# Kernel optimization log

Hardware: AMD Instinct MI355X
Metric: run time of the kernel (lower is better)

Reference implementation:

```python
import jax, jax.numpy as jnp
import numpy as np

N = 50000      # nodes
E = 500000     # edges (includes N self-loops)
DIN = 512
DOUT = 256
NEG_SLOPE = 0.01  # torch nn.LeakyReLU default


def setup_inputs() -> dict:
    key = jax.random.key(0)
    k1, k2, k3, k4, k5 = jax.random.split(key, 5)
    x = jax.random.normal(k1, (N, DIN), dtype=jnp.float32)
    # xavier_normal_ with gain=1.414
    std_W = 1.414 * np.sqrt(2.0 / (DIN + DOUT))
    W = jax.random.normal(k2, (DIN, DOUT), dtype=jnp.float32) * std_W
    std_a = 1.414 * np.sqrt(2.0 / (1 + 2 * DOUT))
    a = jax.random.normal(k3, (2 * DOUT,), dtype=jnp.float32) * std_a
    # first N edges are self-loops so every row-sum is nonzero
    loops = jnp.arange(N, dtype=jnp.int32)
    edge_src = jnp.concatenate([loops, jax.random.randint(k4, (E - N,), 0, N, dtype=jnp.int32)])
    edge_dst = jnp.concatenate([loops, jax.random.randint(k5, (E - N,), 0, N, dtype=jnp.int32)])
    return {"x": x, "W": W, "a": a, "edge_src": edge_src, "edge_dst": edge_dst}


def reference(x, W, a, edge_src, edge_dst):
    n = x.shape[0]
    d = W.shape[1]
    h = x @ W  # [N, DOUT]
    # a . [h_src ; h_dst] decomposed per-node, then gathered per-edge
    s_src = h @ a[:d]   # [N]
    s_dst = h @ a[d:]   # [N]
    score = s_src[edge_src] + s_dst[edge_dst]          # [E]
    e = jnp.exp(-jax.nn.leaky_relu(score, NEG_SLOPE))  # [E]
    # sparse softmax denominator: spmm(edge, e, ones) == segment sum over src
    e_rowsum = jax.ops.segment_sum(e, edge_src, num_segments=n)            # [N]
    # numerator: spmm(edge, e, h) == sum_j e_ij * h_j per row i
    h_prime = jax.ops.segment_sum(e[:, None] * h[edge_dst], edge_src, num_segments=n)  # [N, DOUT]
    h_prime = h_prime / e_rowsum[:, None]
    return jax.nn.elu(h_prime)  # concat=True branch
```

## Files before the change

kernel.cpp:

```cpp
#include <hip/hip_runtime.h>
#include <math.h>

#define DIN 512
#define DOUT 256
#define NEG_SLOPE 0.01f

typedef __attribute__((ext_vector_type(8))) short bf16x8;
typedef __attribute__((ext_vector_type(4))) float f32x4;
typedef __attribute__((ext_vector_type(4))) unsigned int u32x4;

__device__ __forceinline__ unsigned short f2bf(float f) {
    unsigned int u = __float_as_uint(f);
    unsigned int r = (u + 0x7FFFu + ((u >> 16) & 1u)) >> 16;
    return (unsigned short)r;
}
__device__ __forceinline__ float bf2f(unsigned short u) {
    return __uint_as_float(((unsigned int)u) << 16);
}
__device__ __forceinline__ unsigned int cvtpk(float lo, float hi) {
    unsigned int r;
    asm("v_cvt_pk_bf16_f32 %0, %1, %2" : "=v"(r) : "v"(lo), "v"(hi));
    return r;
}

__global__ void prep(const float* __restrict__ W, unsigned short* __restrict__ Bp,
                     int* __restrict__ deg, float* __restrict__ s_src,
                     float* __restrict__ s_dst, int N) {
    int t = blockIdx.x * blockDim.x + threadIdx.x;
    if (t < (DIN / 32) * (DOUT / 16) * 64) {
        int lane = t & 63;
        int cg = (t >> 6) & 15;
        int ks = t >> 10;
        int l15 = lane & 15, g = lane >> 4;
        int col = cg * 16 + l15;
        int k0 = ks * 32 + g * 8;
        ushort4 lo, hi;
        lo.x = f2bf(W[(size_t)(k0 + 0) * DOUT + col]);
        lo.y = f2bf(W[(size_t)(k0 + 1) * DOUT + col]);
        lo.z = f2bf(W[(size_t)(k0 + 2) * DOUT + col]);
        lo.w = f2bf(W[(size_t)(k0 + 3) * DOUT + col]);
        hi.x = f2bf(W[(size_t)(k0 + 4) * DOUT + col]);
        hi.y = f2bf(W[(size_t)(k0 + 5) * DOUT + col]);
        hi.z = f2bf(W[(size_t)(k0 + 6) * DOUT + col]);
        hi.w = f2bf(W[(size_t)(k0 + 7) * DOUT + col]);
        *(ushort4*)(Bp + (size_t)t * 8) = lo;
        *(ushort4*)(Bp + (size_t)t * 8 + 4) = hi;
    }
    if (t < N) { deg[t] = 0; s_src[t] = 0.f; s_dst[t] = 0.f; }
}

__global__ __launch_bounds__(64, 2) void gemm_k(const float* __restrict__ x,
                                                const unsigned short* __restrict__ Bp,
                                                unsigned short* __restrict__ hb,
                                                const float* __restrict__ av,
                                                float* __restrict__ s_src,
                                                float* __restrict__ s_dst, int M) {
    const int lane = threadIdx.x;
    const int l15 = lane & 15;
    const int g = lane >> 4;
    const int m0 = blockIdx.x * 32;

    int r0 = min(m0 + l15, M - 1);
    int r1 = min(m0 + 16 + l15, M - 1);
    const float* pA0 = x + (size_t)r0 * DIN + g * 8;
    const float* pA1 = x + (size_t)r1 * DIN + g * 8;
    const unsigned short* pB = Bp + (size_t)lane * 8;

    f32x4 acc[2][16] = {};

#pragma unroll
    for (int ks = 0; ks < DIN / 32; ++ks) {
        f32x4 a00 = *(const f32x4*)(pA0 + ks * 32);
        f32x4 a01 = *(const f32x4*)(pA0 + ks * 32 + 4);
        f32x4 a10 = *(const f32x4*)(pA1 + ks * 32);
        f32x4 a11 = *(const f32x4*)(pA1 + ks * 32 + 4);
        u32x4 p;
        p.x = cvtpk(a00.x, a00.y); p.y = cvtpk(a00.z, a00.w);
        p.z = cvtpk(a01.x, a01.y); p.w = cvtpk(a01.z, a01.w);
        bf16x8 af0 = *(bf16x8*)&p;
        u32x4 q;
        q.x = cvtpk(a10.x, a10.y); q.y = cvtpk(a10.z, a10.w);
        q.z = cvtpk(a11.x, a11.y); q.w = cvtpk(a11.z, a11.w);
        bf16x8 af1 = *(bf16x8*)&q;
        const unsigned short* pBks = pB + (size_t)ks * 16 * 512;
#pragma unroll
        for (int cg = 0; cg < 16; ++cg) {
            bf16x8 bfr = *(const bf16x8*)(pBks + (size_t)cg * 512);
            acc[0][cg] = __builtin_amdgcn_mfma_f32_16x16x32_bf16(af0, bfr, acc[0][cg], 0, 0, 0);
            acc[1][cg] = __builtin_amdgcn_mfma_f32_16x16x32_bf16(af1, bfr, acc[1][cg], 0, 0, 0);
        }
    }

    float as_[16], ad_[16];
#pragma unroll
    for (int cg = 0; cg < 16; ++cg) {
        int col = cg * 16 + l15;
        as_[cg] = av[col];
        ad_[cg] = av[DOUT + col];
    }
#pragma unroll
    for (int rf = 0; rf < 2; ++rf) {
#pragma unroll
        for (int j = 0; j < 4; ++j) {
            int row = m0 + rf * 16 + g * 4 + j;
            float ps = 0.f, pd = 0.f;
#pragma unroll
            for (int cg = 0; cg < 16; ++cg) {
                float v = acc[rf][cg][j];
                ps += v * as_[cg];
                pd += v * ad_[cg];
            }
#pragma unroll
            for (int off = 1; off < 16; off <<= 1) {
                ps += __shfl_xor(ps, off);
                pd += __shfl_xor(pd, off);
            }
            if (row < M) {
#pragma unroll
                for (int cg = 0; cg < 16; ++cg)
                    hb[(size_t)row * DOUT + cg * 16 + l15] = f2bf(acc[rf][cg][j]);
                if (l15 == 0) {
                    atomicAdd(&s_src[row], ps);
                    atomicAdd(&s_dst[row], pd);
                }
            }
        }
    }
}

__global__ void hist_k(const int* __restrict__ src, int* __restrict__ deg, int E) {
    int i = blockIdx.x * blockDim.x + threadIdx.x;
    if (i < E) atomicAdd(&deg[src[i]], 1);
}

__global__ __launch_bounds__(256) void block_sum(const int* __restrict__ deg, int* __restrict__ bsum, int N) {
    __shared__ int wsum[4];
    int b = blockIdx.x, t = threadIdx.x;
    int idx = b * 1024 + t * 4;
    int s = 0;
    if (idx + 3 < N) {
        int4 v = *(const int4*)(deg + idx);
        s = v.x + v.y + v.z + v.w;
    } else {
        for (int i = 0; i < 4; i++) if (idx + i < N) s += deg[idx + i];
    }
#pragma unroll
    for (int off = 32; off > 0; off >>= 1) s += __shfl_xor(s, off);
    if ((t & 63) == 0) wsum[t >> 6] = s;
    __syncthreads();
    if (t == 0) bsum[b] = wsum[0] + wsum[1] + wsum[2] + wsum[3];
}

__global__ void scan_tops(const int* __restrict__ bsum, int* __restrict__ boff,
                          int* __restrict__ rowptr, int nb, int N, int E) {
    int t = threadIdx.x;
    int v = (t < nb) ? bsum[t] : 0;
    int x = v;
#pragma unroll
    for (int off = 1; off < 64; off <<= 1) {
        int y = __shfl_up(x, off);
        if (t >= off) x += y;
    }
    if (t < nb) boff[t] = x - v;
    if (t == 0) rowptr[N] = E;
}

__global__ __launch_bounds__(256) void scan_blk(const int* __restrict__ deg, const int* __restrict__ boff,
                                                int* __restrict__ rowptr, int* __restrict__ cursor, int N) {
    __shared__ int wsum[4];
    int b = blockIdx.x, t = threadIdx.x;
    int idx = b * 1024 + t * 4;
    int v0 = 0, v1 = 0, v2 = 0, v3 = 0;
    if (idx + 3 < N) {
        int4 v = *(const int4*)(deg + idx);
        v0 = v.x; v1 = v.y; v2 = v.z; v3 = v.w;
    } else if (idx < N) {
        v0 = deg[idx];
        if (idx + 1 < N) v1 = deg[idx + 1];
        if (idx + 2 < N) v2 = deg[idx + 2];
    }
    int s = v0 + v1 + v2 + v3;
    int lane = t & 63, wid = t >> 6;
    int x = s;
#pragma unroll
    for (int off = 1; off < 64; off <<= 1) {
        int y = __shfl_up(x, off);
        if (lane >= off) x += y;
    }
    if (lane == 63) wsum[wid] = x;
    __syncthreads();
    int add = boff[b];
    for (int ww = 0; ww < wid; ++ww) add += wsum[ww];
    int e0 = add + x - s;
    int e1 = e0 + v0, e2 = e1 + v1, e3 = e2 + v2;
    if (idx < N)     { rowptr[idx] = e0;     cursor[idx] = e0; }
    if (idx + 1 < N) { rowptr[idx + 1] = e1; cursor[idx + 1] = e1; }
    if (idx + 2 < N) { rowptr[idx + 2] = e2; cursor[idx + 2] = e2; }
    if (idx + 3 < N) { rowptr[idx + 3] = e3; cursor[idx + 3] = e3; }
}

__global__ void edge_k(const int* __restrict__ src, const int* __restrict__ dst,
                       const float* __restrict__ s_src, const float* __restrict__ s_dst,
                       int* __restrict__ cursor, int2* __restrict__ csr, int E) {
    int i = blockIdx.x * blockDim.x + threadIdx.x;
    if (i >= E) return;
    int s = src[i], d = dst[i];
    float sc = s_src[s] + s_dst[d];
    float lrv = sc > 0.f ? sc : NEG_SLOPE * sc;
    float ev = __expf(-lrv);
    int pos = atomicAdd(&cursor[s], 1);
    csr[pos] = make_int2(d, __float_as_int(ev));
}

__global__ __launch_bounds__(256) void gather_k(const unsigned short* __restrict__ hb,
                                                const int* __restrict__ rowptr,
                                                const int2* __restrict__ csr,
                                                float* __restrict__ out, int N) {
    int gt = blockIdx.x * blockDim.x + threadIdx.x;
    int w = gt >> 6;
    int lane = threadIdx.x & 63;
    if (w >= N) return;
    int s0 = rowptr[w], s1 = rowptr[w + 1];
    float a0 = 0.f, a1 = 0.f, a2 = 0.f, a3 = 0.f, rs = 0.f;
    for (int base = s0; base < s1; base += 64) {
        int cnt = min(64, s1 - base);
        int dv = 0; float ev = 0.f;
        if (lane < cnt) {
            int2 p = csr[base + lane];
            dv = p.x; ev = __int_as_float(p.y);
        }
        int jj = 0;
        for (; jj + 4 <= cnt; jj += 4) {
            int d0 = __shfl(dv, jj), d1 = __shfl(dv, jj + 1), d2 = __shfl(dv, jj + 2), d3 = __shfl(dv, jj + 3);
            float e0 = __shfl(ev, jj), e1 = __shfl(ev, jj + 1), e2 = __shfl(ev, jj + 2), e3 = __shfl(ev, jj + 3);
            ushort4 h0 = *(const ushort4*)(hb + (size_t)d0 * DOUT + lane * 4);
            ushort4 h1 = *(const ushort4*)(hb + (size_t)d1 * DOUT + lane * 4);
            ushort4 h2 = *(const ushort4*)(hb + (size_t)d2 * DOUT + lane * 4);
            ushort4 h3 = *(const ushort4*)(hb + (size_t)d3 * DOUT + lane * 4);
            a0 += e0 * bf2f(h0.x) + e1 * bf2f(h1.x) + e2 * bf2f(h2.x) + e3 * bf2f(h3.x);
            a1 += e0 * bf2f(h0.y) + e1 * bf2f(h1.y) + e2 * bf2f(h2.y) + e3 * bf2f(h3.y);
            a2 += e0 * bf2f(h0.z) + e1 * bf2f(h1.z) + e2 * bf2f(h2.z) + e3 * bf2f(h3.z);
            a3 += e0 * bf2f(h0.w) + e1 * bf2f(h1.w) + e2 * bf2f(h2.w) + e3 * bf2f(h3.w);
            rs += e0 + e1 + e2 + e3;
        }
        for (; jj < cnt; ++jj) {
            int d0 = __shfl(dv, jj);
            float e0 = __shfl(ev, jj);
            ushort4 h0 = *(const ushort4*)(hb + (size_t)d0 * DOUT + lane * 4);
            a0 += e0 * bf2f(h0.x);
            a1 += e0 * bf2f(h0.y);
            a2 += e0 * bf2f(h0.z);
            a3 += e0 * bf2f(h0.w);
            rs += e0;
        }
    }
    float inv = 1.f / rs;
    float4 v;
    v.x = a0 * inv; v.y = a1 * inv; v.z = a2 * inv; v.w = a3 * inv;
    v.x = v.x > 0.f ? v.x : __expf(v.x) - 1.f;
    v.y = v.y > 0.f ? v.y : __expf(v.y) - 1.f;
    v.z = v.z > 0.f ? v.z : __expf(v.z) - 1.f;
    v.w = v.w > 0.f ? v.w : __expf(v.w) - 1.f;
    *(float4*)(out + (size_t)w * DOUT + lane * 4) = v;
}

extern "C" void kernel_launch(void* const* d_in, const int* in_sizes, int n_in,
                              void* d_out, int out_size, void* d_ws, size_t ws_size,
                              hipStream_t stream) {
    const float* x = (const float*)d_in[0];
    const float* W = (const float*)d_in[1];
    const float* a = (const float*)d_in[2];
    const int* edge_src = (const int*)d_in[3];
    const int* edge_dst = (const int*)d_in[4];

    const int N = in_sizes[0] / DIN;
    const int E = in_sizes[3];
    const int nb = (N + 1023) / 1024;

    char* ws = (char*)d_ws;
    size_t off = 0;
    auto alloc = [&](size_t bytes) {
        void* p = ws + off;
        off += (bytes + 15) & ~(size_t)15;
        return p;
    };
    unsigned short* hb = (unsigned short*)alloc((size_t)N * DOUT * 2);
    unsigned short* Bp = (unsigned short*)alloc((size_t)DIN * DOUT * 2);
    int* rowptr = (int*)alloc((size_t)(N + 1) * 4);
    int* deg = (int*)alloc((size_t)N * 4);
    int* cursor = (int*)alloc((size_t)N * 4);
    float* s_src = (float*)alloc((size_t)N * 4);
    float* s_dst = (float*)alloc((size_t)N * 4);
    int2* csr = (int2*)alloc((size_t)E * 8);
    int* bsum = (int*)alloc((size_t)nb * 4);
    int* boff = (int*)alloc((size_t)nb * 4);
    (void)ws_size;

    float* out = (float*)d_out;

    prep<<<(N + 255) / 256, 256, 0, stream>>>(W, Bp, deg, s_src, s_dst, N);
    hist_k<<<(E + 255) / 256, 256, 0, stream>>>(edge_src, deg, E);
    gemm_k<<<(N + 31) / 32, 64, 0, stream>>>(x, Bp, hb, a, s_src, s_dst, N);
    block_sum<<<nb, 256, 0, stream>>>(deg, bsum, N);
    scan_tops<<<1, 64, 0, stream>>>(bsum, boff, rowptr, nb, N, E);
    scan_blk<<<nb, 256, 0, stream>>>(deg, boff, rowptr, cursor, N);
    edge_k<<<(E + 255) / 256, 256, 0, stream>>>(edge_src, edge_dst, s_src, s_dst,
                                                cursor, csr, E);
    gather_k<<<(N + 3) / 4, 256, 0, stream>>>(hb, rowptr, csr, out, N);
}
```

Baseline: 149.2 us.

## Preload all A fragments and double-buffer B loads in GEMM kernel

Loads the whole 32-row A tile from x up front and converts it to bf16 fragments held in registers. B fragments are software-pipelined: the next k-step's 16 B vectors load while the MFMAs for the current step run. Launch bounds drop to one wave per SIMD so the larger register footprint fits. The aim is to hide global load latency behind MFMA work, at the cost of lower occupancy and possible register spills.

```diff
diff --git a/kernel.cpp b/kernel.cpp
--- a/kernel.cpp
+++ b/kernel.cpp
@@ -49,7 +49,7 @@
     if (t < N) { deg[t] = 0; s_src[t] = 0.f; s_dst[t] = 0.f; }
 }
 
-__global__ __launch_bounds__(64, 2) void gemm_k(const float* __restrict__ x,
+__global__ __launch_bounds__(64, 1) void gemm_k(const float* __restrict__ x,
                                                 const unsigned short* __restrict__ Bp,
                                                 unsigned short* __restrict__ hb,
                                                 const float* __restrict__ av,
@@ -66,28 +66,54 @@
     const float* pA1 = x + (size_t)r1 * DIN + g * 8;
     const unsigned short* pB = Bp + (size_t)lane * 8;
 
+    bf16x8 af0[16], af1[16];
+    {
+        f32x4 ra[16], rb[16];
+#pragma unroll
+        for (int ks = 0; ks < 16; ++ks) {
+            ra[ks] = *(const f32x4*)(pA0 + ks * 32);
+            rb[ks] = *(const f32x4*)(pA0 + ks * 32 + 4);
+        }
+#pragma unroll
+        for (int ks = 0; ks < 16; ++ks) {
+            u32x4 p;
+            p.x = cvtpk(ra[ks].x, ra[ks].y); p.y = cvtpk(ra[ks].z, ra[ks].w);
+            p.z = cvtpk(rb[ks].x, rb[ks].y); p.w = cvtpk(rb[ks].z, rb[ks].w);
+            af0[ks] = *(bf16x8*)&p;
+        }
+#pragma unroll
+        for (int ks = 0; ks < 16; ++ks) {
+            ra[ks] = *(const f32x4*)(pA1 + ks * 32);
+            rb[ks] = *(const f32x4*)(pA1 + ks * 32 + 4);
+        }
+#pragma unroll
+        for (int ks = 0; ks < 16; ++ks) {
+            u32x4 p;
+            p.x = cvtpk(ra[ks].x, ra[ks].y); p.y = cvtpk(ra[ks].z, ra[ks].w);
+            p.z = cvtpk(rb[ks].x, rb[ks].y); p.w = cvtpk(rb[ks].z, rb[ks].w);
+            af1[ks] = *(bf16x8*)&p;
+        }
+    }
+
     f32x4 acc[2][16] = {};
-
-#pragma unroll
-    for (int ks = 0; ks < DIN / 32; ++ks) {
-        f32x4 a00 = *(const f32x4*)(pA0 + ks * 32);
-        f32x4 a01 = *(const f32x4*)(pA0 + ks * 32 + 4);
-        f32x4 a10 = *(const f32x4*)(pA1 + ks * 32);
-        f32x4 a11 = *(const f32x4*)(pA1 + ks * 32 + 4);
-        u32x4 p;
-        p.x = cvtpk(a00.x, a00.y); p.y = cvtpk(a00.z, a00.w);
-        p.z = cvtpk(a01.x, a01.y); p.w = cvtpk(a01.z, a01.w);
-        bf16x8 af0 = *(bf16x8*)&p;
-        u32x4 q;
-        q.x = cvtpk(a10.x, a10.y); q.y = cvtpk(a10.z, a10.w);
-        q.z = cvtpk(a11.x, a11.y); q.w = cvtpk(a11.z, a11.w);
-        bf16x8 af1 = *(bf16x8*)&q;
-        const unsigned short* pBks = pB + (size_t)ks * 16 * 512;
+    bf16x8 bbuf[2][16];
+#pragma unroll
+    for (int cg = 0; cg < 16; ++cg)
+        bbuf[0][cg] = *(const bf16x8*)(pB + (size_t)cg * 512);
+#pragma unroll
+    for (int ks = 0; ks < 16; ++ks) {
+        const int cur = ks & 1;
+        const int nxt = cur ^ 1;
+        if (ks < 15) {
+            const unsigned short* pBn = pB + (size_t)(ks + 1) * 16 * 512;
+#pragma unroll
+            for (int cg = 0; cg < 16; ++cg)
+                bbuf[nxt][cg] = *(const bf16x8*)(pBn + (size_t)cg * 512);
+        }
 #pragma unroll
         for (int cg = 0; cg < 16; ++cg) {
-            bf16x8 bfr = *(const bf16x8*)(pBks + (size_t)cg * 512);
-            acc[0][cg] = __builtin_amdgcn_mfma_f32_16x16x32_bf16(af0, bfr, acc[0][cg], 0, 0, 0);
-            acc[1][cg] = __builtin_amdgcn_mfma_f32_16x16x32_bf16(af1, bfr, acc[1][cg], 0, 0, 0);
+            acc[0][cg] = __builtin_amdgcn_mfma_f32_16x16x32_bf16(af0[ks], bbuf[cur][cg], acc[0][cg], 0, 0, 0);
+            acc[1][cg] = __builtin_amdgcn_mfma_f32_16x16x32_bf16(af1[ks], bbuf[cur][cg], acc[1][cg], 0, 0, 0);
         }
     }
 
```

Measured after the change: 178.2 us. +19.5%, slower.

## Split GEMM output columns across two blocks and double-buffer operand loads

Applied to the files above, without the earlier changes.

The GEMM kernel now launches a 2D grid where each block computes half of the 256 output columns, halving accumulator registers and doubling the number of blocks. The K loop also prefetches the next slice of A and B into register double-buffers so loads overlap the MFMAs. In exchange, each x row is read and converted twice, once per column half. The score dot products still combine correctly through the existing atomic adds.

```diff
diff --git a/kernel.cpp b/kernel.cpp
--- a/kernel.cpp
+++ b/kernel.cpp
@@ -59,42 +59,66 @@
     const int l15 = lane & 15;
     const int g = lane >> 4;
     const int m0 = blockIdx.x * 32;
+    const int half = blockIdx.y;
 
     int r0 = min(m0 + l15, M - 1);
     int r1 = min(m0 + 16 + l15, M - 1);
     const float* pA0 = x + (size_t)r0 * DIN + g * 8;
     const float* pA1 = x + (size_t)r1 * DIN + g * 8;
-    const unsigned short* pB = Bp + (size_t)lane * 8;
-
-    f32x4 acc[2][16] = {};
-
-#pragma unroll
-    for (int ks = 0; ks < DIN / 32; ++ks) {
-        f32x4 a00 = *(const f32x4*)(pA0 + ks * 32);
-        f32x4 a01 = *(const f32x4*)(pA0 + ks * 32 + 4);
-        f32x4 a10 = *(const f32x4*)(pA1 + ks * 32);
-        f32x4 a11 = *(const f32x4*)(pA1 + ks * 32 + 4);
+    const unsigned short* pB = Bp + ((size_t)(half * 8) * 64 + lane) * 8;
+
+    f32x4 acc[2][8] = {};
+    f32x4 abuf[2][4];
+    bf16x8 bbuf[2][8];
+
+#pragma unroll
+    for (int i = 0; i < 2; ++i) {
+        abuf[0][2 * i] = *(const f32x4*)((i ? pA1 : pA0));
+        abuf[0][2 * i + 1] = *(const f32x4*)((i ? pA1 : pA0) + 4);
+    }
+#pragma unroll
+    for (int cg = 0; cg < 8; ++cg)
+        bbuf[0][cg] = *(const bf16x8*)(pB + (size_t)cg * 512);
+
+#pragma unroll
+    for (int ks = 0; ks < 16; ++ks) {
+        const int cur = ks & 1;
+        const int nxt = cur ^ 1;
+        if (ks < 15) {
+            const float* qA0 = pA0 + (ks + 1) * 32;
+            const float* qA1 = pA1 + (ks + 1) * 32;
+            abuf[nxt][0] = *(const f32x4*)qA0;
+            abuf[nxt][1] = *(const f32x4*)(qA0 + 4);
+            abuf[nxt][2] = *(const f32x4*)qA1;
+            abuf[nxt][3] = *(const f32x4*)(qA1 + 4);
+            const unsigned short* pBn = pB + (size_t)(ks + 1) * 16 * 512;
+#pragma unroll
+            for (int cg = 0; cg < 8; ++cg)
+                bbuf[nxt][cg] = *(const bf16x8*)(pBn + (size_t)cg * 512);
+        }
         u32x4 p;
-        p.x = cvtpk(a00.x, a00.y); p.y = cvtpk(a00.z, a00.w);
-        p.z = cvtpk(a01.x, a01.y); p.w = cvtpk(a01.z, a01.w);
+        p.x = cvtpk(abuf[cur][0].x, abuf[cur][0].y);
+        p.y = cvtpk(abuf[cur][0].z, abuf[cur][0].w);
+        p.z = cvtpk(abuf[cur][1].x, abuf[cur][1].y);
+        p.w = cvtpk(abuf[cur][1].z, abuf[cur][1].w);
         bf16x8 af0 = *(bf16x8*)&p;
         u32x4 q;
-        q.x = cvtpk(a10.x, a10.y); q.y = cvtpk(a10.z, a10.w);
-        q.z = cvtpk(a11.x, a11.y); q.w = cvtpk(a11.z, a11.w);
+        q.x = cvtpk(abuf[cur][2].x, abuf[cur][2].y);
+        q.y = cvtpk(abuf[cur][2].z, abuf[cur][2].w);
+        q.z = cvtpk(abuf[cur][3].x, abuf[cur][3].y);
+        q.w = cvtpk(abuf[cur][3].z, abuf[cur][3].w);
         bf16x8 af1 = *(bf16x8*)&q;
-        const unsigned short* pBks = pB + (size_t)ks * 16 * 512;
-#pragma unroll
-        for (int cg = 0; cg < 16; ++cg) {
-            bf16x8 bfr = *(const bf16x8*)(pBks + (size_t)cg * 512);
-            acc[0][cg] = __builtin_amdgcn_mfma_f32_16x16x32_bf16(af0, bfr, acc[0][cg], 0, 0, 0);
-            acc[1][cg] = __builtin_amdgcn_mfma_f32_16x16x32_bf16(af1, bfr, acc[1][cg], 0, 0, 0);
-        }
-    }
-
-    float as_[16], ad_[16];
-#pragma unroll
-    for (int cg = 0; cg < 16; ++cg) {
-        int col = cg * 16 + l15;
+#pragma unroll
+        for (int cg = 0; cg < 8; ++cg) {
+            acc[0][cg] = __builtin_amdgcn_mfma_f32_16x16x32_bf16(af0, bbuf[cur][cg], acc[0][cg], 0, 0, 0);
+            acc[1][cg] = __builtin_amdgcn_mfma_f32_16x16x32_bf16(af1, bbuf[cur][cg], acc[1][cg], 0, 0, 0);
+        }
+    }
+
+    float as_[8], ad_[8];
+#pragma unroll
+    for (int cg = 0; cg < 8; ++cg) {
+        int col = half * 128 + cg * 16 + l15;
         as_[cg] = av[col];
         ad_[cg] = av[DOUT + col];
     }
@@ -105,7 +129,7 @@
             int row = m0 + rf * 16 + g * 4 + j;
             float ps = 0.f, pd = 0.f;
 #pragma unroll
-            for (int cg = 0; cg < 16; ++cg) {
+            for (int cg = 0; cg < 8; ++cg) {
                 float v = acc[rf][cg][j];
                 ps += v * as_[cg];
                 pd += v * ad_[cg];
@@ -117,8 +141,8 @@
             }
             if (row < M) {
 #pragma unroll
-                for (int cg = 0; cg < 16; ++cg)
-                    hb[(size_t)row * DOUT + cg * 16 + l15] = f2bf(acc[rf][cg][j]);
+                for (int cg = 0; cg < 8; ++cg)
+                    hb[(size_t)row * DOUT + half * 128 + cg * 16 + l15] = f2bf(acc[rf][cg][j]);
                 if (l15 == 0) {
                     atomicAdd(&s_src[row], ps);
                     atomicAdd(&s_dst[row], pd);
@@ -300,7 +324,8 @@
 
     prep<<<(N + 255) / 256, 256, 0, stream>>>(W, Bp, deg, s_src, s_dst, N);
     hist_k<<<(E + 255) / 256, 256, 0, stream>>>(edge_src, deg, E);
-    gemm_k<<<(N + 31) / 32, 64, 0, stream>>>(x, Bp, hb, a, s_src, s_dst, N);
+    dim3 ggrid((N + 31) / 32, 2);
+    gemm_k<<<ggrid, 64, 0, stream>>>(x, Bp, hb, a, s_src, s_dst, N);
     block_sum<<<nb, 256, 0, stream>>>(deg, bsum, N);
     scan_tops<<<1, 64, 0, stream>>>(bsum, boff, rowptr, nb, N, E);
     scan_blk<<<nb, 256, 0, stream>>>(deg, boff, rowptr, cursor, N);
```

Result: slower. 174.9 us (+17.3%).
